# Optimization experiments

Hardware: AMD Instinct MI355X
Metric: run time of the kernel (lower is better)

## Reference

```python
import jax, jax.numpy as jnp
import numpy as np

MAPP = jnp.array([0.5, 1.0, 1.5, 2.0], dtype=jnp.float32)  # magnitude constellation (len = one_hot_len)


def setup_inputs() -> dict:
    key = jax.random.key(0)
    ks = jax.random.split(key, 20)
    B, BL, SM = 512, 256, 8
    S = BL + SM            # sym_len = 264
    V, Z, OH = 128, 1024, 4
    inp = {}
    inp["l"] = 0
    inp["x_mag"] = jax.random.uniform(ks[0], (1, B, S), jnp.float32)
    inp["x_mag_oh"] = jax.random.normal(ks[1], (B, S * OH), jnp.float32)
    inp["v"] = jax.random.normal(ks[2], (B, V), jnp.float32)
    inp["x_phase"] = jax.random.normal(ks[3], (1, B, S), jnp.float32)
    inp["y_e"] = jax.random.normal(ks[4], (B, BL), jnp.float32)
    inp["y_o"] = jax.random.normal(ks[5], (B, BL), jnp.float32)
    inp["Psi_e"] = jax.random.normal(ks[6], (B, 2 * BL, 2 * S), jnp.float32) * 0.1
    inp["Psi_o"] = jax.random.normal(ks[7], (B, 2 * BL, 2 * S), jnp.float32) * 0.1
    # Linear params, std=0.01 as in torch init
    inp["W1"] = jax.random.normal(ks[8], (Z, S + V), jnp.float32) * 0.01
    inp["b1"] = jax.random.normal(ks[9], (Z,), jnp.float32) * 0.01
    inp["W2"] = jax.random.normal(ks[10], (S * OH, Z), jnp.float32) * 0.01
    inp["b2"] = jax.random.normal(ks[11], (S * OH,), jnp.float32) * 0.01
    inp["W3"] = jax.random.normal(ks[12], (V, Z), jnp.float32) * 0.01
    inp["b3"] = jax.random.normal(ks[13], (V,), jnp.float32) * 0.01
    inp["d1"] = jax.random.uniform(ks[14], (1,), jnp.float32)
    inp["d2"] = jax.random.uniform(ks[15], (1,), jnp.float32)
    inp["d3"] = jax.random.uniform(ks[16], (1,), jnp.float32)
    inp["d4"] = jax.random.uniform(ks[17], (1,), jnp.float32)
    return inp


def reference(l, x_mag, x_mag_oh, v, x_phase, y_e, y_o, Psi_e, Psi_o,
              W1, b1, W2, b2, W3, b3, d1, d2, d3, d4):
    B, S = x_phase.shape[1], x_phase.shape[2]
    BL = y_e.shape[1]
    mag, ph = x_mag[-1], x_phase[-1]          # [B,S]
    c, s = jnp.cos(ph), jnp.sin(ph)
    x = jnp.concatenate([mag * c, mag * s], axis=-1)  # [B,2S]

    def A_and_sql(Psi):
        # Psi: [B, 2*BL, 2*S]
        Px = jnp.einsum('bms,bs->bm', Psi, x)         # [B, 2*BL]
        a, b_ = Px[:, :BL], Px[:, BL:]
        # Psi^T @ blockdiag(a,b) == row-scale Psi (avoids diag_embed+bmm):
        # M[b,j,i] = Psi[b,j,i]*a[b,j] + Psi[b,BL+j,i]*b[b,j]  -> [B, BL, 2S]
        M = Psi[:, :BL, :] * a[:, :, None] + Psi[:, BL:, :] * b_[:, :, None]
        # jacobian @ (Psi^T D) == cos/sin row-scaling of the two S-halves:
        A = (c[:, :, None] * jnp.swapaxes(M[:, :, :S], 1, 2)
             + s[:, :, None] * jnp.swapaxes(M[:, :, S:], 1, 2))  # [B, S, BL]
        sql = a * a + b_ * b_                          # [B, BL]
        return A, sql

    A_e, sql_e = A_and_sql(Psi_e)
    A_o, sql_o = A_and_sql(Psi_o)
    mv = lambda A, y: jnp.einsum('bsk,bk->bs', A, y)
    # NOTE: original code uses delta2 for the A_o@y_o term (delta3 unused) -- kept faithful.
    q = (mag - d1 * mv(A_e, y_e) + d2 * mv(A_e, sql_e)
         - d2 * mv(A_o, y_o) + d4 * mv(A_o, sql_o))    # [B,S]

    z = jax.nn.relu(jnp.concatenate([q, v], axis=1) @ W1.T + b1)   # [B,Z]
    x_mag_oh_new = x_mag_oh + z @ W2.T + b2                        # [B,S*OH]
    # oh_2_sym: softmax over one-hot dim, expectation over constellation
    sym = jax.nn.softmax(x_mag_oh_new.reshape(B, S, -1), axis=-1) @ MAPP  # [B,S]
    x_mag_new = jnp.concatenate([x_mag, sym[None]], axis=0)
    v_new = v + z @ W3.T + b3
    return (x_mag_new, x_mag_oh_new, v_new)
```

## Files before the change

### kernel.cpp

```cpp
#include <hip/hip_runtime.h>
#include <stdint.h>

#define S_     264
#define BL_    256
#define TWO_S  528
#define TWO_BL 512
#define B_     512
#define V_     128
#define NQ     392
#define Z_     1024
#define N2_    1056
#define NTOT   1184

#define CHUNK_F4 1056
#define NCHUNK   64

__device__ __forceinline__ void gload_lds16(const void* g, void* l) {
    __builtin_amdgcn_global_load_lds(
        (const __attribute__((address_space(1))) uint32_t*)g,
        (__attribute__((address_space(3))) uint32_t*)l, 16, 0, 0);
}

__device__ __forceinline__ void stage_chunk(const float4* Pg, int chunk,
                                            float4* dst, int tid) {
    const float4* lo = Pg + (size_t)(chunk * 4) * 132;
    const float4* hi = Pg + (size_t)(chunk * 4 + BL_) * 132;
    #pragma unroll
    for (int r = 0; r < 4; ++r) {
        const int i = r * 256 + tid;
        const float4* g = (i < 528) ? (lo + i) : (hi + (i - 528));
        gload_lds16((const void*)g, (void*)(dst + i));
    }
    if (tid < 32) {
        const int i = 1024 + tid;
        gload_lds16((const void*)(hi + (i - 528)), (void*)(dst + i));
    }
}

__global__ __launch_bounds__(256, 4) void k_psi(
    const float* __restrict__ x_mag, const float* __restrict__ x_phase,
    const float* __restrict__ y_e, const float* __restrict__ y_o,
    const float* __restrict__ Psi_e, const float* __restrict__ Psi_o,
    const float* __restrict__ d1, const float* __restrict__ d2,
    const float* __restrict__ d4,
    float* __restrict__ contrib, float* __restrict__ out0)
{
    const int tid = threadIdx.x;
    const int b   = blockIdx.x >> 1;
    const int psi = blockIdx.x & 1;
    const float* Psi = psi ? Psi_o : Psi_e;
    const float* yv  = psi ? y_o  : y_e;
    const float coefY = psi ? -d2[0] : -d1[0];
    const float coefS = psi ?  d4[0] :  d2[0];

    __shared__ float4 bufA[CHUNK_F4];
    __shared__ float4 bufB[CHUNK_F4];
    __shared__ float4 xs4[132];
    __shared__ float  cs[S_], sn[S_];
    __shared__ float  gys[BL_];

    float* xs = (float*)xs4;

    for (int s = tid; s < S_; s += 256) {
        float mag = x_mag[(size_t)b * S_ + s];
        float ph  = x_phase[(size_t)b * S_ + s];
        float c = cosf(ph), si = sinf(ph);
        cs[s] = c; sn[s] = si;
        xs[s]      = mag * c;
        xs[S_ + s] = mag * si;
        if (psi == 0) out0[(size_t)b * S_ + s] = mag;
    }
    gys[tid] = coefY * yv[(size_t)b * BL_ + tid];

    const float4* Pg = (const float4*)(Psi + (size_t)b * TWO_BL * TWO_S);

    stage_chunk(Pg, 0, bufA, tid);
    __syncthreads();

    const int wave = tid >> 6, lane = tid & 63;
    const float4 f4z = {0.f, 0.f, 0.f, 0.f};

    float4 x0 = xs4[lane];
    float4 x1 = xs4[lane + 64];
    float4 x2 = (lane < 4) ? xs4[lane + 128] : f4z;

    float4 u0 = f4z, u1 = f4z, u2 = f4z;

    for (int c = 0; c < NCHUNK; ++c) {
        float4* cur = (c & 1) ? bufB : bufA;
        float4* nxt = (c & 1) ? bufA : bufB;
        if (c + 1 < NCHUNK) stage_chunk(Pg, c + 1, nxt, tid);

        const float4* bl = cur + wave * 132;
        const float4* bh = bl + 528;
        float4 l0 = bl[lane], l1 = bl[lane + 64];
        float4 h0 = bh[lane], h1 = bh[lane + 64];
        float4 l2 = f4z, h2 = f4z;
        if (lane < 4) { l2 = bl[lane + 128]; h2 = bh[lane + 128]; }

        float a  = l0.x*x0.x + l0.y*x0.y + l0.z*x0.z + l0.w*x0.w
                 + l1.x*x1.x + l1.y*x1.y + l1.z*x1.z + l1.w*x1.w
                 + l2.x*x2.x + l2.y*x2.y + l2.z*x2.z + l2.w*x2.w;
        float bb = h0.x*x0.x + h0.y*x0.y + h0.z*x0.z + h0.w*x0.w
                 + h1.x*x1.x + h1.y*x1.y + h1.z*x1.z + h1.w*x1.w
                 + h2.x*x2.x + h2.y*x2.y + h2.z*x2.z + h2.w*x2.w;
        #pragma unroll
        for (int off = 32; off; off >>= 1) {
            a  += __shfl_xor(a, off);
            bb += __shfl_xor(bb, off);
        }

        const float g  = gys[c * 4 + wave] + coefS * (a * a + bb * bb);
        const float wl = a * g, wh = bb * g;

        u0.x += l0.x*wl + h0.x*wh;  u0.y += l0.y*wl + h0.y*wh;
        u0.z += l0.z*wl + h0.z*wh;  u0.w += l0.w*wl + h0.w*wh;
        u1.x += l1.x*wl + h1.x*wh;  u1.y += l1.y*wl + h1.y*wh;
        u1.z += l1.z*wl + h1.z*wh;  u1.w += l1.w*wl + h1.w*wh;
        u2.x += l2.x*wl + h2.x*wh;  u2.y += l2.y*wl + h2.y*wh;
        u2.z += l2.z*wl + h2.z*wh;  u2.w += l2.w*wl + h2.w*wh;

        __syncthreads();
    }

    float4* redU4 = bufA;
    redU4[wave * 132 + lane]      = u0;
    redU4[wave * 132 + 64 + lane] = u1;
    if (lane < 4) redU4[wave * 132 + 128 + lane] = u2;
    __syncthreads();

    const float* redU = (const float*)bufA;
    float* outp = contrib + (size_t)(b * 2 + psi) * S_;
    for (int s = tid; s < S_; s += 256) {
        float ul = redU[0*TWO_S + s]       + redU[1*TWO_S + s]
                 + redU[2*TWO_S + s]       + redU[3*TWO_S + s];
        float uh = redU[0*TWO_S + S_ + s]  + redU[1*TWO_S + S_ + s]
                 + redU[2*TWO_S + S_ + s]  + redU[3*TWO_S + S_ + s];
        outp[s] = cs[s] * ul + sn[s] * uh;
    }
}

__global__ __launch_bounds__(256) void k_gemm1(
    const float* __restrict__ x_mag, const float* __restrict__ contrib,
    const float* __restrict__ v, const float* __restrict__ W1,
    const float* __restrict__ b1, float* __restrict__ z)
{
    const int tid = threadIdx.x;
    const int m0  = blockIdx.x * 32;
    const int n0  = blockIdx.y * 64;
    const int trow = (tid >> 4) * 2;
    const int tcol = (tid & 15) * 4;

    __shared__ float As[32][36];
    __shared__ float Ws[32][68];

    float acc[2][4] = {};

    const int krA  = tid >> 3;
    const int kkA  = (tid & 7) * 4;

    for (int kc = 0; kc < NQ; kc += 32) {
        {
            const int arow = m0 + krA;
            const int gk = kc + kkA;
            float4 vv = {0.f, 0.f, 0.f, 0.f};
            if (gk < S_) {
                float4 xm = *(const float4*)&x_mag[(size_t)arow * S_ + gk];
                float4 ce = *(const float4*)&contrib[(size_t)(arow * 2) * S_ + gk];
                float4 co = *(const float4*)&contrib[(size_t)(arow * 2 + 1) * S_ + gk];
                vv.x = xm.x + ce.x + co.x; vv.y = xm.y + ce.y + co.y;
                vv.z = xm.z + ce.z + co.z; vv.w = xm.w + ce.w + co.w;
            } else if (gk < NQ) {
                vv = *(const float4*)&v[(size_t)arow * V_ + (gk - S_)];
            }
            As[kkA + 0][krA] = vv.x; As[kkA + 1][krA] = vv.y;
            As[kkA + 2][krA] = vv.z; As[kkA + 3][krA] = vv.w;
        }
        for (int i = tid; i < 512; i += 256) {
            const int r  = i >> 3;
            const int j4 = (i & 7) * 4;
            const int gk = kc + j4;
            float4 vv = {0.f, 0.f, 0.f, 0.f};
            if (gk < NQ)
                vv = *(const float4*)&W1[(size_t)(n0 + r) * NQ + gk];
            Ws[j4 + 0][r] = vv.x; Ws[j4 + 1][r] = vv.y;
            Ws[j4 + 2][r] = vv.z; Ws[j4 + 3][r] = vv.w;
        }
        __syncthreads();

        #pragma unroll
        for (int k = 0; k < 32; ++k) {
            float2 a2 = *(const float2*)&As[k][trow];
            float4 w4 = *(const float4*)&Ws[k][tcol];
            acc[0][0] += a2.x * w4.x; acc[0][1] += a2.x * w4.y;
            acc[0][2] += a2.x * w4.z; acc[0][3] += a2.x * w4.w;
            acc[1][0] += a2.y * w4.x; acc[1][1] += a2.y * w4.y;
            acc[1][2] += a2.y * w4.z; acc[1][3] += a2.y * w4.w;
        }
        __syncthreads();
    }

    #pragma unroll
    for (int i = 0; i < 2; ++i) {
        const int row = m0 + trow + i;
        const int col = n0 + tcol;
        float4 r;
        r.x = fmaxf(acc[i][0] + b1[col + 0], 0.f);
        r.y = fmaxf(acc[i][1] + b1[col + 1], 0.f);
        r.z = fmaxf(acc[i][2] + b1[col + 2], 0.f);
        r.w = fmaxf(acc[i][3] + b1[col + 3], 0.f);
        *(float4*)&z[(size_t)row * Z_ + col] = r;
    }
}

__global__ __launch_bounds__(256) void k_gemm23(
    const float* __restrict__ z,
    const float* __restrict__ W2, const float* __restrict__ b2,
    const float* __restrict__ oh,
    const float* __restrict__ W3, const float* __restrict__ b3,
    const float* __restrict__ v,
    float* __restrict__ out_oh, float* __restrict__ out_v,
    float* __restrict__ out0)
{
    const int tid = threadIdx.x;
    const int m0  = blockIdx.x * 32;
    const int n0  = blockIdx.y * 64;
    const int trow = (tid >> 4) * 2;
    const int tcol = (tid & 15) * 4;

    __shared__ float As[32][36];
    __shared__ float Ws[32][68];

    float acc[2][4] = {};

    const int krA = tid >> 3;
    const int kkA = (tid & 7) * 4;

    for (int kc = 0; kc < Z_; kc += 32) {
        {
            float4 vv = *(const float4*)&z[(size_t)(m0 + krA) * Z_ + kc + kkA];
            As[kkA + 0][krA] = vv.x; As[kkA + 1][krA] = vv.y;
            As[kkA + 2][krA] = vv.z; As[kkA + 3][krA] = vv.w;
        }
        for (int i = tid; i < 512; i += 256) {
            const int r  = i >> 3;
            const int j4 = (i & 7) * 4;
            const int wrow = n0 + r;
            float4 vv = {0.f, 0.f, 0.f, 0.f};
            if (wrow < NTOT) {
                const float* wp = (wrow < N2_)
                    ? (W2 + (size_t)wrow * Z_)
                    : (W3 + (size_t)(wrow - N2_) * Z_);
                vv = *(const float4*)&wp[kc + j4];
            }
            Ws[j4 + 0][r] = vv.x; Ws[j4 + 1][r] = vv.y;
            Ws[j4 + 2][r] = vv.z; Ws[j4 + 3][r] = vv.w;
        }
        __syncthreads();

        #pragma unroll
        for (int k = 0; k < 32; ++k) {
            float2 a2 = *(const float2*)&As[k][trow];
            float4 w4 = *(const float4*)&Ws[k][tcol];
            acc[0][0] += a2.x * w4.x; acc[0][1] += a2.x * w4.y;
            acc[0][2] += a2.x * w4.z; acc[0][3] += a2.x * w4.w;
            acc[1][0] += a2.y * w4.x; acc[1][1] += a2.y * w4.y;
            acc[1][2] += a2.y * w4.z; acc[1][3] += a2.y * w4.w;
        }
        __syncthreads();
    }

    #pragma unroll
    for (int i = 0; i < 2; ++i) {
        const int row = m0 + trow + i;
        const int col = n0 + tcol;
        if (col < N2_) {
            float4 ad = *(const float4*)&oh[(size_t)row * N2_ + col];
            float4 r;
            r.x = acc[i][0] + b2[col + 0] + ad.x;
            r.y = acc[i][1] + b2[col + 1] + ad.y;
            r.z = acc[i][2] + b2[col + 2] + ad.z;
            r.w = acc[i][3] + b2[col + 3] + ad.w;
            *(float4*)&out_oh[(size_t)row * N2_ + col] = r;
            float m  = fmaxf(fmaxf(r.x, r.y), fmaxf(r.z, r.w));
            float e0 = expf(r.x - m), e1 = expf(r.y - m);
            float e2 = expf(r.z - m), e3 = expf(r.w - m);
            float sum = e0 + e1 + e2 + e3;
            float sym = (0.5f * e0 + 1.0f * e1 + 1.5f * e2 + 2.0f * e3) / sum;
            out0[(size_t)B_ * S_ + (size_t)row * S_ + (col >> 2)] = sym;
        } else if (col < NTOT) {
            const int c3 = col - N2_;
            float4 ad = *(const float4*)&v[(size_t)row * V_ + c3];
            float4 r;
            r.x = acc[i][0] + b3[c3 + 0] + ad.x;
            r.y = acc[i][1] + b3[c3 + 1] + ad.y;
            r.z = acc[i][2] + b3[c3 + 2] + ad.z;
            r.w = acc[i][3] + b3[c3 + 3] + ad.w;
            *(float4*)&out_v[(size_t)row * V_ + c3] = r;
        }
    }
}

extern "C" void kernel_launch(void* const* d_in, const int* in_sizes, int n_in,
                              void* d_out, int out_size, void* d_ws, size_t ws_size,
                              hipStream_t stream)
{
    const float* x_mag    = (const float*)d_in[1];
    const float* x_mag_oh = (const float*)d_in[2];
    const float* v        = (const float*)d_in[3];
    const float* x_phase  = (const float*)d_in[4];
    const float* y_e      = (const float*)d_in[5];
    const float* y_o      = (const float*)d_in[6];
    const float* Psi_e    = (const float*)d_in[7];
    const float* Psi_o    = (const float*)d_in[8];
    const float* W1       = (const float*)d_in[9];
    const float* b1       = (const float*)d_in[10];
    const float* W2       = (const float*)d_in[11];
    const float* b2       = (const float*)d_in[12];
    const float* W3       = (const float*)d_in[13];
    const float* b3       = (const float*)d_in[14];
    const float* d1       = (const float*)d_in[15];
    const float* d2       = (const float*)d_in[16];
    const float* d4       = (const float*)d_in[18];

    float* ws      = (float*)d_ws;
    float* contrib = ws;
    float* z       = contrib + 1024 * S_;

    float* out0   = (float*)d_out;
    float* out_oh = out0 + 2 * B_ * S_;
    float* out_v  = out_oh + B_ * N2_;

    k_psi<<<dim3(B_ * 2), dim3(256), 0, stream>>>(
        x_mag, x_phase, y_e, y_o, Psi_e, Psi_o, d1, d2, d4, contrib, out0);

    k_gemm1<<<dim3(16, 16), dim3(256), 0, stream>>>(
        x_mag, contrib, v, W1, b1, z);

    k_gemm23<<<dim3(16, 19), dim3(256), 0, stream>>>(
        z, W2, b2, x_mag_oh, W3, b3, v, out_oh, out_v, out0);
}
```

Baseline: 299.6 us.

## Split Psi row range across two smaller blocks per batch-psi pair

The Psi kernel now launches four 128-thread blocks per batch item, one per (psi, row-half) pair, instead of two 256-thread blocks, and halves the LDS staging buffers. Each block writes its own partial contribution, and the first GEMM sums four partials instead of two. The aim is more blocks, more resident waves per CU and better latency hiding in this memory-bound Psi read. In exchange, each block now recomputes the x vector and its cos/sin values, and twice as much partial data is written and read back.

Result: no change. 304.0 us (+1.5%).

```diff
diff --git a/kernel.cpp b/kernel.cpp
--- a/kernel.cpp
+++ b/kernel.cpp
@@ -12,8 +12,7 @@
 #define N2_    1056
 #define NTOT   1184
 
-#define CHUNK_F4 1056
-#define NCHUNK   64
+#define CH_F4  528
 
 __device__ __forceinline__ void gload_lds16(const void* g, void* l) {
     __builtin_amdgcn_global_load_lds(
@@ -21,60 +20,62 @@
         (__attribute__((address_space(3))) uint32_t*)l, 16, 0, 0);
 }
 
-__device__ __forceinline__ void stage_chunk(const float4* Pg, int chunk,
-                                            float4* dst, int tid) {
-    const float4* lo = Pg + (size_t)(chunk * 4) * 132;
-    const float4* hi = Pg + (size_t)(chunk * 4 + BL_) * 132;
+__device__ __forceinline__ void stage2(const float4* Pg, int half, int c,
+                                       float4* buf, int tid) {
     #pragma unroll
     for (int r = 0; r < 4; ++r) {
-        const int i = r * 256 + tid;
-        const float4* g = (i < 528) ? (lo + i) : (hi + (i - 528));
-        gload_lds16((const void*)g, (void*)(dst + i));
-    }
-    if (tid < 32) {
-        const int i = 1024 + tid;
-        gload_lds16((const void*)(hi + (i - 528)), (void*)(dst + i));
-    }
-}
-
-__global__ __launch_bounds__(256, 4) void k_psi(
+        const int i  = r * 128 + tid;
+        const int pi = (i >= 264) ? 1 : 0;
+        const int o  = i - pi * 264;
+        const int m  = half * 128 + c * 2 + pi;
+        const float4* src = Pg + (size_t)((o < 132) ? (m * 132 + o)
+                                                    : ((m + BL_) * 132 + (o - 132)));
+        gload_lds16((const void*)src, (void*)(buf + i));
+    }
+    if (tid < 16) {
+        const int i = 512 + tid;
+        const int m = half * 128 + c * 2 + 1;
+        const float4* src = Pg + (size_t)((m + BL_) * 132 + (i - 264 - 132));
+        gload_lds16((const void*)src, (void*)(buf + i));
+    }
+}
+
+__global__ __launch_bounds__(128) void k_psi(
     const float* __restrict__ x_mag, const float* __restrict__ x_phase,
     const float* __restrict__ y_e, const float* __restrict__ y_o,
     const float* __restrict__ Psi_e, const float* __restrict__ Psi_o,
     const float* __restrict__ d1, const float* __restrict__ d2,
     const float* __restrict__ d4,
-    float* __restrict__ contrib, float* __restrict__ out0)
+    float* __restrict__ contribP, float* __restrict__ out0)
 {
-    const int tid = threadIdx.x;
-    const int b   = blockIdx.x >> 1;
-    const int psi = blockIdx.x & 1;
+    const int tid  = threadIdx.x;
+    const int b    = blockIdx.x >> 2;
+    const int psi  = (blockIdx.x >> 1) & 1;
+    const int half = blockIdx.x & 1;
     const float* Psi = psi ? Psi_o : Psi_e;
     const float* yv  = psi ? y_o  : y_e;
     const float coefY = psi ? -d2[0] : -d1[0];
     const float coefS = psi ?  d4[0] :  d2[0];
 
-    __shared__ float4 bufA[CHUNK_F4];
-    __shared__ float4 bufB[CHUNK_F4];
+    __shared__ float4 bufA[CH_F4];
+    __shared__ float4 bufB[CH_F4];
     __shared__ float4 xs4[132];
-    __shared__ float  cs[S_], sn[S_];
-    __shared__ float  gys[BL_];
+    __shared__ float  gys[128];
 
     float* xs = (float*)xs4;
 
-    for (int s = tid; s < S_; s += 256) {
+    for (int s = tid; s < S_; s += 128) {
         float mag = x_mag[(size_t)b * S_ + s];
         float ph  = x_phase[(size_t)b * S_ + s];
-        float c = cosf(ph), si = sinf(ph);
-        cs[s] = c; sn[s] = si;
-        xs[s]      = mag * c;
-        xs[S_ + s] = mag * si;
-        if (psi == 0) out0[(size_t)b * S_ + s] = mag;
-    }
-    gys[tid] = coefY * yv[(size_t)b * BL_ + tid];
+        xs[s]      = mag * cosf(ph);
+        xs[S_ + s] = mag * sinf(ph);
+        if (psi == 0 && half == 0) out0[(size_t)b * S_ + s] = mag;
+    }
+    gys[tid] = coefY * yv[(size_t)b * BL_ + half * 128 + tid];
 
     const float4* Pg = (const float4*)(Psi + (size_t)b * TWO_BL * TWO_S);
 
-    stage_chunk(Pg, 0, bufA, tid);
+    stage2(Pg, half, 0, bufA, tid);
     __syncthreads();
 
     const int wave = tid >> 6, lane = tid & 63;
@@ -86,13 +87,13 @@
 
     float4 u0 = f4z, u1 = f4z, u2 = f4z;
 
-    for (int c = 0; c < NCHUNK; ++c) {
+    for (int c = 0; c < 64; ++c) {
         float4* cur = (c & 1) ? bufB : bufA;
         float4* nxt = (c & 1) ? bufA : bufB;
-        if (c + 1 < NCHUNK) stage_chunk(Pg, c + 1, nxt, tid);
-
-        const float4* bl = cur + wave * 132;
-        const float4* bh = bl + 528;
+        if (c + 1 < 64) stage2(Pg, half, c + 1, nxt, tid);
+
+        const float4* bl = cur + wave * 264;
+        const float4* bh = bl + 132;
         float4 l0 = bl[lane], l1 = bl[lane + 64];
         float4 h0 = bh[lane], h1 = bh[lane + 64];
         float4 l2 = f4z, h2 = f4z;
@@ -110,7 +111,7 @@
             bb += __shfl_xor(bb, off);
         }
 
-        const float g  = gys[c * 4 + wave] + coefS * (a * a + bb * bb);
+        const float g  = gys[c * 2 + wave] + coefS * (a * a + bb * bb);
         const float wl = a * g, wh = bb * g;
 
         u0.x += l0.x*wl + h0.x*wh;  u0.y += l0.y*wl + h0.y*wh;
@@ -123,25 +124,23 @@
         __syncthreads();
     }
 
-    float4* redU4 = bufA;
-    redU4[wave * 132 + lane]      = u0;
-    redU4[wave * 132 + 64 + lane] = u1;
-    if (lane < 4) redU4[wave * 132 + 128 + lane] = u2;
+    bufA[wave * 132 + lane]      = u0;
+    bufA[wave * 132 + 64 + lane] = u1;
+    if (lane < 4) bufA[wave * 132 + 128 + lane] = u2;
     __syncthreads();
 
-    const float* redU = (const float*)bufA;
-    float* outp = contrib + (size_t)(b * 2 + psi) * S_;
-    for (int s = tid; s < S_; s += 256) {
-        float ul = redU[0*TWO_S + s]       + redU[1*TWO_S + s]
-                 + redU[2*TWO_S + s]       + redU[3*TWO_S + s];
-        float uh = redU[0*TWO_S + S_ + s]  + redU[1*TWO_S + S_ + s]
-                 + redU[2*TWO_S + S_ + s]  + redU[3*TWO_S + S_ + s];
-        outp[s] = cs[s] * ul + sn[s] * uh;
+    const float* red = (const float*)bufA;
+    float* outp = contribP + (size_t)blockIdx.x * S_;
+    for (int s = tid; s < S_; s += 128) {
+        float ul = red[s]       + red[528 + s];
+        float uh = red[S_ + s]  + red[528 + S_ + s];
+        float ph = x_phase[(size_t)b * S_ + s];
+        outp[s] = cosf(ph) * ul + sinf(ph) * uh;
     }
 }
 
 __global__ __launch_bounds__(256) void k_gemm1(
-    const float* __restrict__ x_mag, const float* __restrict__ contrib,
+    const float* __restrict__ x_mag, const float* __restrict__ contribP,
     const float* __restrict__ v, const float* __restrict__ W1,
     const float* __restrict__ b1, float* __restrict__ z)
 {
@@ -166,10 +165,15 @@
             float4 vv = {0.f, 0.f, 0.f, 0.f};
             if (gk < S_) {
                 float4 xm = *(const float4*)&x_mag[(size_t)arow * S_ + gk];
-                float4 ce = *(const float4*)&contrib[(size_t)(arow * 2) * S_ + gk];
-                float4 co = *(const float4*)&contrib[(size_t)(arow * 2 + 1) * S_ + gk];
-                vv.x = xm.x + ce.x + co.x; vv.y = xm.y + ce.y + co.y;
-                vv.z = xm.z + ce.z + co.z; vv.w = xm.w + ce.w + co.w;
+                const float* cb = contribP + (size_t)(arow * 4) * S_ + gk;
+                float4 c0 = *(const float4*)(cb);
+                float4 c1 = *(const float4*)(cb + S_);
+                float4 c2 = *(const float4*)(cb + 2 * S_);
+                float4 c3 = *(const float4*)(cb + 3 * S_);
+                vv.x = xm.x + c0.x + c1.x + c2.x + c3.x;
+                vv.y = xm.y + c0.y + c1.y + c2.y + c3.y;
+                vv.z = xm.z + c0.z + c1.z + c2.z + c3.z;
+                vv.w = xm.w + c0.w + c1.w + c2.w + c3.w;
             } else if (gk < NQ) {
                 vv = *(const float4*)&v[(size_t)arow * V_ + (gk - S_)];
             }
@@ -323,19 +327,19 @@
     const float* d2       = (const float*)d_in[16];
     const float* d4       = (const float*)d_in[18];
 
-    float* ws      = (float*)d_ws;
-    float* contrib = ws;
-    float* z       = contrib + 1024 * S_;
+    float* ws       = (float*)d_ws;
+    float* contribP = ws;
+    float* z        = contribP + 2048 * S_;
 
     float* out0   = (float*)d_out;
     float* out_oh = out0 + 2 * B_ * S_;
     float* out_v  = out_oh + B_ * N2_;
 
-    k_psi<<<dim3(B_ * 2), dim3(256), 0, stream>>>(
-        x_mag, x_phase, y_e, y_o, Psi_e, Psi_o, d1, d2, d4, contrib, out0);
+    k_psi<<<dim3(B_ * 4), dim3(128), 0, stream>>>(
+        x_mag, x_phase, y_e, y_o, Psi_e, Psi_o, d1, d2, d4, contribP, out0);
 
     k_gemm1<<<dim3(16, 16), dim3(256), 0, stream>>>(
-        x_mag, contrib, v, W1, b1, z);
+        x_mag, contribP, v, W1, b1, z);
 
     k_gemm23<<<dim3(16, 19), dim3(256), 0, stream>>>(
         z, W2, b2, x_mag_oh, W3, b3, v, out_oh, out_v, out0);
```
